# Performance work log

Measured on AMD Instinct MI355X. Metric: run time of the kernel, lower is better.

Reference implementation:

```python
import jax, jax.numpy as jnp
import numpy as np

DIM = 1024


def setup_inputs() -> dict:
    key = jax.random.key(0)
    ks = jax.random.split(key, 9)
    s = 1.0 / np.sqrt(DIM)
    x = jax.random.normal(ks[0], (4, 4096, DIM), dtype=jnp.float32)
    Wq = jax.random.uniform(ks[1], (DIM, DIM), jnp.float32, -s, s)
    bq = jax.random.uniform(ks[2], (DIM,), jnp.float32, -s, s)
    Wk = jax.random.uniform(ks[3], (DIM, DIM), jnp.float32, -s, s)
    bk = jax.random.uniform(ks[4], (DIM,), jnp.float32, -s, s)
    Wv = jax.random.uniform(ks[5], (DIM, DIM), jnp.float32, -s, s)
    bv = jax.random.uniform(ks[6], (DIM,), jnp.float32, -s, s)
    Wo = jax.random.uniform(ks[7], (DIM, DIM), jnp.float32, -s, s)
    bo = jax.random.uniform(ks[8], (DIM,), jnp.float32, -s, s)
    return {"x": x, "Wq": Wq, "bq": bq, "Wk": Wk, "bk": bk,
            "Wv": Wv, "bv": bv, "Wo": Wo, "bo": bo}


def reference(x, Wq, bq, Wk, bk, Wv, bv, Wo, bo):
    # x: [B, N, C]; weights stored as [C, C] (torch Linear applies x @ W.T,
    # here we store W already transposed so x @ W matches).
    scale = x.shape[-1] ** (-0.5)
    q = x @ Wq + bq                                  # [B, N, C]
    k = x @ Wk + bk
    v = x @ Wv + bv
    scores = jnp.einsum('bnc,bmc->bnm', q, k) * scale  # [B, N, N]
    attn = jax.nn.softmax(scores, axis=-1)
    out = jnp.einsum('bnm,bmc->bnc', attn, v)          # [B, N, C]
    return out @ Wo + bo
```

## Files before the change

### kernel.cpp

```cpp
#include <hip/hip_runtime.h>
#include <hip/hip_bf16.h>
#include <stdint.h>

typedef __bf16 bf16_8 __attribute__((ext_vector_type(8)));
typedef float  f32x4  __attribute__((ext_vector_type(4)));

#define GLL(g, l) __builtin_amdgcn_global_load_lds(                         \
    (__attribute__((address_space(1))) void*)(g),                           \
    (__attribute__((address_space(3))) void*)(l), 16, 0, 0)

__global__ void sniff_dtype(const uint32_t* __restrict__ x, uint32_t* __restrict__ flag)
{
    uint32_t w = x[threadIdx.x];
    uint32_t e = (w >> 23) & 0xFF;
    int isf32 = (e >= 100 && e <= 145) ? 1 : 0;
    unsigned long long m = __ballot(isf32);
    if (threadIdx.x == 0) *flag = (__popcll(m) >= 48) ? 1u : 0u;
}

__global__ __launch_bounds__(256)
void convert_to_bf16(const void* __restrict__ in, long elemOff,
                     __bf16* __restrict__ out, long n, const uint32_t* __restrict__ flag)
{
    long i = ((long)blockIdx.x * 256 + threadIdx.x) * 8;
    if (i >= n) return;
    bf16_8 o;
    if (*flag) {
        const float* p = (const float*)in + elemOff + i;
        float4 a = *(const float4*)p;
        float4 b = *(const float4*)(p + 4);
        o[0]=(__bf16)a.x; o[1]=(__bf16)a.y; o[2]=(__bf16)a.z; o[3]=(__bf16)a.w;
        o[4]=(__bf16)b.x; o[5]=(__bf16)b.y; o[6]=(__bf16)b.z; o[7]=(__bf16)b.w;
    } else {
        o = *(const bf16_8*)((const __bf16*)in + elemOff + i);
    }
    *(bf16_8*)(out + i) = o;
}

__global__ __launch_bounds__(256)
void convT_w(const void* __restrict__ W, __bf16* __restrict__ WT,
             const uint32_t* __restrict__ flag)
{
    __shared__ __bf16 tile[64][72];
    const int bc = blockIdx.x * 64, br = blockIdx.y * 64;
    const int c = threadIdx.x & 63, r0 = threadIdx.x >> 6;
    const bool f32 = (*flag != 0);
#pragma unroll
    for (int i = 0; i < 16; i++) {
        int r = i * 4 + r0;
        long idx = (long)(br + r) * 1024 + bc + c;
        float v = f32 ? ((const float*)W)[idx] : (float)((const __bf16*)W)[idx];
        tile[r][c] = (__bf16)v;
    }
    __syncthreads();
#pragma unroll
    for (int i = 0; i < 16; i++) {
        int r = i * 4 + r0;
        WT[(long)(bc + r) * 1024 + br + c] = tile[c][r];
    }
}

template<int BN_T, int OUT_MODE, bool HAS_BIAS>
__global__ __launch_bounds__(256)
void gemm_bt(const __bf16* __restrict__ A, int lda,
             const __bf16* __restrict__ BT, int ldb,
             void* __restrict__ C, int ldc,
             const __bf16* __restrict__ bias,
             int M, int N, int K, float scale)
{
    constexpr int NT    = (BN_T == 128) ? 4 : 2;
    constexpr int BHALF = BN_T * 32;
    __shared__ __align__(16) __bf16 As[2 * 128 * 32];
    __shared__ __align__(16) __bf16 Bs[2 * BHALF];

    const int t    = threadIdx.x;
    const int wave = t >> 6;
    const int lane = t & 63;
    const int quad = lane >> 4;
    const int lrow = lane & 15;
    const int wm   = wave >> 1;
    const int wn   = wave & 1;
    const long m0  = (long)blockIdx.y * 128;
    const long n0  = (long)blockIdx.x * BN_T;

    const int sr = lane >> 2;
    const int sc = (lane & 3) ^ ((lane >> 3) & 3);

    const __bf16* aSrc = A + (m0 + wave * 32 + sr) * (long)lda + sc * 8;
    const __bf16* bSrc = (BN_T == 128)
        ? BT + (n0 + wave * 32 + sr) * (long)ldb + sc * 8
        : BT + (n0 + wave * 16 + sr) * (long)ldb + sc * 8;
    __bf16* aDst = As + wave * 1024;
    __bf16* bDst = Bs + wave * (BN_T == 128 ? 1024 : 512);
    const long a16 = 16L * lda, b16 = 16L * ldb;

    f32x4 zero4 = {0.f, 0.f, 0.f, 0.f};
    f32x4 acc[4][NT];
#pragma unroll
    for (int mt = 0; mt < 4; mt++)
#pragma unroll
        for (int nt = 0; nt < NT; nt++) acc[mt][nt] = zero4;

    const int sl = (lrow >> 1) & 3;

    for (int k0 = 0; k0 < K; k0 += 64) {
        GLL(aSrc, aDst);
        GLL(aSrc + a16, aDst + 512);
        GLL(bSrc, bDst);
        if (BN_T == 128) GLL(bSrc + b16, bDst + 512);
        GLL(aSrc + 32, aDst + 4096);
        GLL(aSrc + a16 + 32, aDst + 4096 + 512);
        GLL(bSrc + 32, bDst + BHALF);
        if (BN_T == 128) GLL(bSrc + b16 + 32, bDst + BHALF + 512);
        aSrc += 64; bSrc += 64;
        __syncthreads();

#pragma unroll
        for (int kk = 0; kk < 2; kk++) {
            bf16_8 af[4], bfr[NT];
#pragma unroll
            for (int mt = 0; mt < 4; mt++)
                af[mt] = *(const bf16_8*)(As + kk * 4096
                           + (wm * 64 + mt * 16 + lrow) * 32 + (quad ^ sl) * 8);
#pragma unroll
            for (int nt = 0; nt < NT; nt++)
                bfr[nt] = *(const bf16_8*)(Bs + kk * BHALF
                           + (wn * (BN_T / 2) + nt * 16 + lrow) * 32 + (quad ^ sl) * 8);

#pragma unroll
            for (int mt = 0; mt < 4; mt++)
#pragma unroll
                for (int nt = 0; nt < NT; nt++)
                    acc[mt][nt] = __builtin_amdgcn_mfma_f32_16x16x32_bf16(
                                      af[mt], bfr[nt], acc[mt][nt], 0, 0, 0);
        }
        __syncthreads();
    }

#pragma unroll
    for (int mt = 0; mt < 4; mt++) {
#pragma unroll
        for (int nt = 0; nt < NT; nt++) {
#pragma unroll
            for (int i = 0; i < 4; i++) {
                long row = m0 + wm * 64 + mt * 16 + quad * 4 + i;
                long col = n0 + wn * (BN_T / 2) + nt * 16 + lrow;
                float v = acc[mt][nt][i] * scale;
                if (HAS_BIAS) v += (float)bias[col];
                if (OUT_MODE == 0)      ((__bf16*)C)[row * (long)ldc + col] = (__bf16)v;
                else if (OUT_MODE == 1) ((__bf16*)C)[col * (long)ldc + row] = (__bf16)v;
                else                    ((float* )C)[row * (long)ldc + col] = v;
            }
        }
    }
}

__global__ __launch_bounds__(256)
void softmax_f32_to_bf16(float* __restrict__ S)
{
    float* srow = S + (long)blockIdx.x * 4096;
    __bf16* prow = (__bf16*)srow;
    const int t  = threadIdx.x;
    const int wv = t >> 6, ln = t & 63;

    float4 vv[4];
    float m = -1e30f;
#pragma unroll
    for (int i = 0; i < 4; i++) {
        vv[i] = ((const float4*)srow)[t + i * 256];
        m = fmaxf(m, fmaxf(fmaxf(vv[i].x, vv[i].y), fmaxf(vv[i].z, vv[i].w)));
    }
#pragma unroll
    for (int o = 32; o; o >>= 1) m = fmaxf(m, __shfl_xor(m, o));
    __shared__ float redm[4];
    if (ln == 0) redm[wv] = m;
    __syncthreads();
    m = fmaxf(fmaxf(redm[0], redm[1]), fmaxf(redm[2], redm[3]));

    const float L2E = 1.4426950408889634f;
    float s = 0.f;
#pragma unroll
    for (int i = 0; i < 4; i++) {
        vv[i].x = exp2f((vv[i].x - m) * L2E);
        vv[i].y = exp2f((vv[i].y - m) * L2E);
        vv[i].z = exp2f((vv[i].z - m) * L2E);
        vv[i].w = exp2f((vv[i].w - m) * L2E);
        s += vv[i].x + vv[i].y + vv[i].z + vv[i].w;
    }
#pragma unroll
    for (int o = 32; o; o >>= 1) s += __shfl_xor(s, o);
    __shared__ float reds[4];
    if (ln == 0) reds[wv] = s;
    __syncthreads();
    s = reds[0] + reds[1] + reds[2] + reds[3];
    float inv = 1.f / s;

    __syncthreads();
#pragma unroll
    for (int i = 0; i < 4; i++) {
        long base = (long)(t + i * 256) * 4;
        prow[base + 0] = (__bf16)(vv[i].x * inv);
        prow[base + 1] = (__bf16)(vv[i].y * inv);
        prow[base + 2] = (__bf16)(vv[i].z * inv);
        prow[base + 3] = (__bf16)(vv[i].w * inv);
    }
}

__global__ void fill_const_f32(float* p, long n, float val)
{
    long i = (long)blockIdx.x * 256 + threadIdx.x;
    if (i < n) p[i] = val;
}

extern "C" void kernel_launch(void* const* d_in, const int* in_sizes, int n_in,
                              void* d_out, int out_size, void* d_ws, size_t ws_size,
                              hipStream_t stream)
{
    const void* x  = d_in[0];
    const void* Wq = d_in[1];
    const void* bq = d_in[2];
    const void* Wk = d_in[3];
    const void* bk = d_in[4];
    const void* Wv = d_in[5];
    const void* bv = d_in[6];
    const void* Wo = d_in[7];
    const void* bo = d_in[8];

    const int  Bb = 4, Nn = 4096, Cc = 1024;
    const long seqB = (long)Nn * Cc;

    auto pad = [](size_t b) { return (b + 255) & ~(size_t)255; };
    const size_t szW    = (size_t)Cc * Cc * 2;
    const size_t szBias = (size_t)Cc * 2;
    const size_t szSeq  = (size_t)seqB * 2;
    const size_t szAo   = (size_t)Bb * seqB * 2;

    const size_t need = pad(256) + 4 * pad(szW) + 4 * pad(szBias)
                      + pad(szAo) + 4 * pad(szSeq);

    dim3 blk(256);

    if (ws_size < need) {
        float val = 3000.0f + (float)(ws_size >> 20);
        fill_const_f32<<<dim3((out_size + 255) / 256), blk, 0, stream>>>(
            (float*)d_out, out_size, val);
        return;
    }

    char* ws = (char*)d_ws;
    size_t off = 0;
    auto alloc = [&](size_t bytes) -> char* { char* p = ws + off; off += pad(bytes); return p; };

    uint32_t* flag = (uint32_t*)alloc(256);
    __bf16* WqT = (__bf16*)alloc(szW);
    __bf16* WkT = (__bf16*)alloc(szW);
    __bf16* WvT = (__bf16*)alloc(szW);
    __bf16* WoT = (__bf16*)alloc(szW);
    __bf16* bqc = (__bf16*)alloc(szBias);
    __bf16* bkc = (__bf16*)alloc(szBias);
    __bf16* bvc = (__bf16*)alloc(szBias);
    __bf16* boc = (__bf16*)alloc(szBias);
    __bf16* ao  = (__bf16*)alloc(szAo);
    __bf16* xc  = (__bf16*)alloc(szSeq);
    __bf16* q   = (__bf16*)alloc(szSeq);
    __bf16* k   = (__bf16*)alloc(szSeq);
    __bf16* vT  = (__bf16*)alloc(szSeq);

    float* S = (float*)d_out;

    sniff_dtype<<<dim3(1), dim3(64), 0, stream>>>((const uint32_t*)x, flag);

    convT_w<<<dim3(16, 16), blk, 0, stream>>>(Wq, WqT, flag);
    convT_w<<<dim3(16, 16), blk, 0, stream>>>(Wk, WkT, flag);
    convT_w<<<dim3(16, 16), blk, 0, stream>>>(Wv, WvT, flag);
    convT_w<<<dim3(16, 16), blk, 0, stream>>>(Wo, WoT, flag);
    convert_to_bf16<<<dim3(1), blk, 0, stream>>>(bq, 0, bqc, Cc, flag);
    convert_to_bf16<<<dim3(1), blk, 0, stream>>>(bk, 0, bkc, Cc, flag);
    convert_to_bf16<<<dim3(1), blk, 0, stream>>>(bv, 0, bvc, Cc, flag);
    convert_to_bf16<<<dim3(1), blk, 0, stream>>>(bo, 0, boc, Cc, flag);

    const float scale = 0.03125f;

    for (int b = 0; b < Bb; b++) {
        convert_to_bf16<<<dim3(seqB / 2048), blk, 0, stream>>>(x, b * seqB, xc, seqB, flag);

        dim3 gProj(Cc / 64, Nn / 128);
        gemm_bt<64, 0, true><<<gProj, blk, 0, stream>>>(xc, Cc, WqT, Cc, q,  Cc, bqc, Nn, Cc, Cc, 1.f);
        gemm_bt<64, 0, true><<<gProj, blk, 0, stream>>>(xc, Cc, WkT, Cc, k,  Cc, bkc, Nn, Cc, Cc, 1.f);
        gemm_bt<64, 1, true><<<gProj, blk, 0, stream>>>(xc, Cc, WvT, Cc, vT, Nn, bvc, Nn, Cc, Cc, 1.f);

        gemm_bt<128, 2, false><<<dim3(Nn / 128, Nn / 128), blk, 0, stream>>>(
            q, Cc, k, Cc, S, Nn, nullptr, Nn, Nn, Cc, scale);

        softmax_f32_to_bf16<<<dim3(Nn), blk, 0, stream>>>(S);

        gemm_bt<64, 0, false><<<dim3(Cc / 64, Nn / 128), blk, 0, stream>>>(
            (const __bf16*)S, 2 * Nn, vT, Nn, ao + b * seqB, Cc, nullptr, Nn, Cc, Nn, 1.f);
    }

    gemm_bt<128, 2, true><<<dim3(Cc / 128, (Bb * Nn) / 128), blk, 0, stream>>>(
        ao, Cc, WoT, Cc, (float*)d_out, Cc, boc, Bb * Nn, Cc, Cc, 1.f);
}
```

Baseline: 954.5 us.

## Batch QKV projections across batch, split-K the PV GEMM, merge setup launches

When the workspace is large enough, x is converted and projected for all four batches in one launch per weight instead of per-batch launches. The attention-times-V GEMM is split into two K halves via blockIdx.z, writing fp32 partials into spare space of the score buffer, then a reduction kernel sums them into bf16. Weight-transpose and bias-convert launches are merged into single launches. This raises grid size and occupancy for the 128x64-tile PV GEMM and cuts launch count, at the cost of extra fp32 traffic for the partials and an added reduction pass.

```diff
diff --git a/kernel.cpp b/kernel.cpp
--- a/kernel.cpp
+++ b/kernel.cpp
@@ -38,9 +38,38 @@
 }
 
 __global__ __launch_bounds__(256)
-void convT_w(const void* __restrict__ W, __bf16* __restrict__ WT,
-             const uint32_t* __restrict__ flag)
-{
+void convert_bias4(const void* b0, const void* b1, const void* b2, const void* b3,
+                   __bf16* o0, __bf16* o1, __bf16* o2, __bf16* o3,
+                   const uint32_t* __restrict__ flag)
+{
+    const void* in = (blockIdx.x == 0) ? b0 : (blockIdx.x == 1) ? b1
+                   : (blockIdx.x == 2) ? b2 : b3;
+    __bf16* out = (blockIdx.x == 0) ? o0 : (blockIdx.x == 1) ? o1
+                : (blockIdx.x == 2) ? o2 : o3;
+    long i = (long)threadIdx.x * 8;
+    if (i >= 1024) return;
+    bf16_8 o;
+    if (*flag) {
+        const float* p = (const float*)in + i;
+        float4 a = *(const float4*)p;
+        float4 b = *(const float4*)(p + 4);
+        o[0]=(__bf16)a.x; o[1]=(__bf16)a.y; o[2]=(__bf16)a.z; o[3]=(__bf16)a.w;
+        o[4]=(__bf16)b.x; o[5]=(__bf16)b.y; o[6]=(__bf16)b.z; o[7]=(__bf16)b.w;
+    } else {
+        o = *(const bf16_8*)((const __bf16*)in + i);
+    }
+    *(bf16_8*)(out + i) = o;
+}
+
+__global__ __launch_bounds__(256)
+void convT_w4(const void* W0, const void* W1, const void* W2, const void* W3,
+              __bf16* T0, __bf16* T1, __bf16* T2, __bf16* T3,
+              const uint32_t* __restrict__ flag)
+{
+    const void* W = (blockIdx.z == 0) ? W0 : (blockIdx.z == 1) ? W1
+                  : (blockIdx.z == 2) ? W2 : W3;
+    __bf16* WT    = (blockIdx.z == 0) ? T0 : (blockIdx.z == 1) ? T1
+                  : (blockIdx.z == 2) ? T2 : T3;
     __shared__ __bf16 tile[64][72];
     const int bc = blockIdx.x * 64, br = blockIdx.y * 64;
     const int c = threadIdx.x & 63, r0 = threadIdx.x >> 6;
@@ -66,7 +95,7 @@
              const __bf16* __restrict__ BT, int ldb,
              void* __restrict__ C, int ldc,
              const __bf16* __restrict__ bias,
-             int M, int N, int K, float scale)
+             int M, int N, int kLen, long zCbytes, float scale)
 {
     constexpr int NT    = (BN_T == 128) ? 4 : 2;
     constexpr int BHALF = BN_T * 32;
@@ -83,6 +112,10 @@
     const long m0  = (long)blockIdx.y * 128;
     const long n0  = (long)blockIdx.x * BN_T;
 
+    A  += (long)blockIdx.z * kLen;
+    BT += (long)blockIdx.z * kLen;
+    C   = (void*)((char*)C + (long)blockIdx.z * zCbytes);
+
     const int sr = lane >> 2;
     const int sc = (lane & 3) ^ ((lane >> 3) & 3);
 
@@ -103,7 +136,7 @@
 
     const int sl = (lrow >> 1) & 3;
 
-    for (int k0 = 0; k0 < K; k0 += 64) {
+    for (int k0 = 0; k0 < kLen; k0 += 64) {
         GLL(aSrc, aDst);
         GLL(aSrc + a16, aDst + 512);
         GLL(bSrc, bDst);
@@ -206,6 +239,21 @@
     }
 }
 
+__global__ __launch_bounds__(256)
+void reduce2_to_bf16(const float* __restrict__ Sf, __bf16* __restrict__ ao)
+{
+    const long i = blockIdx.x;
+    const float* p = Sf + 4096 * i + 2048;
+    const int t = threadIdx.x;
+    float4 a = ((const float4*)p)[t];
+    float4 b = ((const float4*)(p + 1024))[t];
+    __bf16* o = ao + i * 1024 + t * 4;
+    o[0] = (__bf16)(a.x + b.x);
+    o[1] = (__bf16)(a.y + b.y);
+    o[2] = (__bf16)(a.z + b.z);
+    o[3] = (__bf16)(a.w + b.w);
+}
+
 __global__ void fill_const_f32(float* p, long n, float val)
 {
     long i = (long)blockIdx.x * 256 + threadIdx.x;
@@ -228,24 +276,28 @@
 
     const int  Bb = 4, Nn = 4096, Cc = 1024;
     const long seqB = (long)Nn * Cc;
+    const long allR = (long)Bb * Nn;
 
     auto pad = [](size_t b) { return (b + 255) & ~(size_t)255; };
     const size_t szW    = (size_t)Cc * Cc * 2;
     const size_t szBias = (size_t)Cc * 2;
     const size_t szSeq  = (size_t)seqB * 2;
-    const size_t szAo   = (size_t)Bb * seqB * 2;
-
-    const size_t need = pad(256) + 4 * pad(szW) + 4 * pad(szBias)
-                      + pad(szAo) + 4 * pad(szSeq);
+    const size_t szAll  = (size_t)allR * Cc * 2;
+
+    const size_t fixed = pad(256) + 4 * pad(szW) + 4 * pad(szBias) + pad(szAll);
+    const size_t needB = fixed + 4 * pad(szSeq);
+    const size_t needA = fixed + 4 * pad(szAll);
 
     dim3 blk(256);
 
-    if (ws_size < need) {
+    if (ws_size < needB) {
         float val = 3000.0f + (float)(ws_size >> 20);
         fill_const_f32<<<dim3((out_size + 255) / 256), blk, 0, stream>>>(
             (float*)d_out, out_size, val);
         return;
     }
+
+    const bool batched = (ws_size >= needA);
 
     char* ws = (char*)d_ws;
     size_t off = 0;
@@ -260,44 +312,56 @@
     __bf16* bkc = (__bf16*)alloc(szBias);
     __bf16* bvc = (__bf16*)alloc(szBias);
     __bf16* boc = (__bf16*)alloc(szBias);
-    __bf16* ao  = (__bf16*)alloc(szAo);
-    __bf16* xc  = (__bf16*)alloc(szSeq);
-    __bf16* q   = (__bf16*)alloc(szSeq);
-    __bf16* k   = (__bf16*)alloc(szSeq);
-    __bf16* vT  = (__bf16*)alloc(szSeq);
+    __bf16* ao  = (__bf16*)alloc(szAll);
+    const size_t tierSz = batched ? szAll : szSeq;
+    __bf16* xc  = (__bf16*)alloc(tierSz);
+    __bf16* q   = (__bf16*)alloc(tierSz);
+    __bf16* k   = (__bf16*)alloc(tierSz);
+    __bf16* vT  = (__bf16*)alloc(tierSz);
 
     float* S = (float*)d_out;
 
     sniff_dtype<<<dim3(1), dim3(64), 0, stream>>>((const uint32_t*)x, flag);
-
-    convT_w<<<dim3(16, 16), blk, 0, stream>>>(Wq, WqT, flag);
-    convT_w<<<dim3(16, 16), blk, 0, stream>>>(Wk, WkT, flag);
-    convT_w<<<dim3(16, 16), blk, 0, stream>>>(Wv, WvT, flag);
-    convT_w<<<dim3(16, 16), blk, 0, stream>>>(Wo, WoT, flag);
-    convert_to_bf16<<<dim3(1), blk, 0, stream>>>(bq, 0, bqc, Cc, flag);
-    convert_to_bf16<<<dim3(1), blk, 0, stream>>>(bk, 0, bkc, Cc, flag);
-    convert_to_bf16<<<dim3(1), blk, 0, stream>>>(bv, 0, bvc, Cc, flag);
-    convert_to_bf16<<<dim3(1), blk, 0, stream>>>(bo, 0, boc, Cc, flag);
+    convT_w4<<<dim3(16, 16, 4), blk, 0, stream>>>(Wq, Wk, Wv, Wo, WqT, WkT, WvT, WoT, flag);
+    convert_bias4<<<dim3(4), blk, 0, stream>>>(bq, bk, bv, bo, bqc, bkc, bvc, boc, flag);
 
     const float scale = 0.03125f;
 
+    if (batched) {
+        convert_to_bf16<<<dim3(allR * Cc / 2048), blk, 0, stream>>>(x, 0, xc, allR * Cc, flag);
+        dim3 gProj(Cc / 64, allR / 128);
+        gemm_bt<64, 0, true><<<gProj, blk, 0, stream>>>(xc, Cc, WqT, Cc, q,  Cc,  bqc, (int)allR, Cc, Cc, 0, 1.f);
+        gemm_bt<64, 0, true><<<gProj, blk, 0, stream>>>(xc, Cc, WkT, Cc, k,  Cc,  bkc, (int)allR, Cc, Cc, 0, 1.f);
+        gemm_bt<64, 1, true><<<gProj, blk, 0, stream>>>(xc, Cc, WvT, Cc, vT, (int)allR, bvc, (int)allR, Cc, Cc, 0, 1.f);
+    }
+
     for (int b = 0; b < Bb; b++) {
-        convert_to_bf16<<<dim3(seqB / 2048), blk, 0, stream>>>(x, b * seqB, xc, seqB, flag);
-
-        dim3 gProj(Cc / 64, Nn / 128);
-        gemm_bt<64, 0, true><<<gProj, blk, 0, stream>>>(xc, Cc, WqT, Cc, q,  Cc, bqc, Nn, Cc, Cc, 1.f);
-        gemm_bt<64, 0, true><<<gProj, blk, 0, stream>>>(xc, Cc, WkT, Cc, k,  Cc, bkc, Nn, Cc, Cc, 1.f);
-        gemm_bt<64, 1, true><<<gProj, blk, 0, stream>>>(xc, Cc, WvT, Cc, vT, Nn, bvc, Nn, Cc, Cc, 1.f);
+        const __bf16 *qb, *kb, *vTb;
+        int ldvT;
+        if (batched) {
+            qb = q + (long)b * seqB;  kb = k + (long)b * seqB;
+            vTb = vT + (long)b * Nn;  ldvT = (int)allR;
+        } else {
+            convert_to_bf16<<<dim3(seqB / 2048), blk, 0, stream>>>(x, b * seqB, xc, seqB, flag);
+            dim3 gProj(Cc / 64, Nn / 128);
+            gemm_bt<64, 0, true><<<gProj, blk, 0, stream>>>(xc, Cc, WqT, Cc, q,  Cc, bqc, Nn, Cc, Cc, 0, 1.f);
+            gemm_bt<64, 0, true><<<gProj, blk, 0, stream>>>(xc, Cc, WkT, Cc, k,  Cc, bkc, Nn, Cc, Cc, 0, 1.f);
+            gemm_bt<64, 1, true><<<gProj, blk, 0, stream>>>(xc, Cc, WvT, Cc, vT, Nn, bvc, Nn, Cc, Cc, 0, 1.f);
+            qb = q; kb = k; vTb = vT; ldvT = Nn;
+        }
 
         gemm_bt<128, 2, false><<<dim3(Nn / 128, Nn / 128), blk, 0, stream>>>(
-            q, Cc, k, Cc, S, Nn, nullptr, Nn, Nn, Cc, scale);
+            qb, Cc, kb, Cc, S, Nn, nullptr, Nn, Nn, Cc, 0, scale);
 
         softmax_f32_to_bf16<<<dim3(Nn), blk, 0, stream>>>(S);
 
-        gemm_bt<64, 0, false><<<dim3(Cc / 64, Nn / 128), blk, 0, stream>>>(
-            (const __bf16*)S, 2 * Nn, vT, Nn, ao + b * seqB, Cc, nullptr, Nn, Cc, Nn, 1.f);
-    }
-
-    gemm_bt<128, 2, true><<<dim3(Cc / 128, (Bb * Nn) / 128), blk, 0, stream>>>(
-        ao, Cc, WoT, Cc, (float*)d_out, Cc, boc, Bb * Nn, Cc, Cc, 1.f);
-}
+        gemm_bt<64, 2, false><<<dim3(Cc / 64, Nn / 128, 2), blk, 0, stream>>>(
+            (const __bf16*)S, 2 * Nn, vTb, ldvT, (float*)S + 2048, Nn,
+            nullptr, Nn, Cc, Nn / 2, 4096 , 1.f);
+
+        reduce2_to_bf16<<<dim3(Nn), blk, 0, stream>>>(S, ao + (long)b * seqB);
+    }
+
+    gemm_bt<128, 2, true><<<dim3(Cc / 128, (int)(allR / 128)), blk, 0, stream>>>(
+        ao, Cc, WoT, Cc, (float*)d_out, Cc, boc, (int)allR, Cc, Cc, 0, 1.f);
+}
```

Result: faster. 911.3 us (-4.5%).
